# Performance work log

Hardware: AMD Instinct MI355X
Metric: run time of the kernel (lower is better)

Reference implementation:

```python
import jax, jax.numpy as jnp
import numpy as np

B, N, D, H = 8, 1024, 768, 12
HD = D // H  # head_dim = 64


def setup_inputs() -> dict:
    key = jax.random.key(0)
    ks = jax.random.split(key, 7)
    s = 1.0 / np.sqrt(D)  # xavier-ish scale for weights
    return {
        "x1": jax.random.normal(ks[0], (B, N, D), dtype=jnp.float32),
        "x2": jax.random.normal(ks[1], (B, N, D), dtype=jnp.float32),
        "Wq": jax.random.normal(ks[2], (D, D), dtype=jnp.float32) * s,
        "Wk": jax.random.normal(ks[3], (D, D), dtype=jnp.float32) * s,
        "Wv": jax.random.normal(ks[4], (D, D), dtype=jnp.float32) * s,
        "Wo": jax.random.normal(ks[5], (D, D), dtype=jnp.float32) * s,
        "bo": jnp.zeros((D,), dtype=jnp.float32),
    }


def _heads(x):
    # (B, N, D) -> (B, H, N, HD)
    return x.reshape(B, -1, H, HD).transpose(0, 2, 1, 3)


def reference(x1, x2, Wq, Wk, Wv, Wo, bo):
    scale = 1.0 / jnp.sqrt(jnp.asarray(HD, x1.dtype))
    q1 = _heads(x1 @ Wq.T)               # (B,H,N,HD)
    k1 = _heads(x1 @ Wk.T)
    v1 = _heads(x1 @ Wv.T)
    k2 = _heads(x2 @ Wk.T)
    v2 = _heads(x2 @ Wv.T)
    kc = jnp.concatenate([k1, k2], axis=2)   # (B,H,2N,HD)
    vc = jnp.concatenate([v1, v2], axis=2)
    attn = jnp.einsum('bhnd,bhmd->bhnm', q1, kc) * scale  # (B,H,N,2N)
    attn = jax.nn.softmax(attn, axis=-1)
    out = jnp.einsum('bhnm,bhmd->bhnd', attn, vc)          # (B,H,N,HD)
    out = out.transpose(0, 2, 1, 3).reshape(B, N, D)
    return out @ Wo.T + bo
```

## Files before the change

kernel.cpp:

```cpp
#include <hip/hip_runtime.h>


typedef __bf16 bf16x8 __attribute__((ext_vector_type(8)));
typedef float  f32x4  __attribute__((ext_vector_type(4)));
typedef unsigned int u32x4 __attribute__((ext_vector_type(4)));
typedef short  s16x4  __attribute__((ext_vector_type(4)));

__device__ __forceinline__ unsigned short bf16bits(float f) {
    return __builtin_bit_cast(unsigned short, (__bf16)f);
}
__device__ __forceinline__ unsigned pk2(float a, float b) {
    return (unsigned)bf16bits(a) | ((unsigned)bf16bits(b) << 16);
}
__device__ __forceinline__ bf16x8 asbf(u32x4 v) {
    return __builtin_bit_cast(bf16x8, v);
}
__device__ __forceinline__ float fexp2(float x) {
#if __has_builtin(__builtin_amdgcn_exp2f)
    return __builtin_amdgcn_exp2f(x);
#else
    return exp2f(x);
#endif
}
__device__ __forceinline__ float frcp(float x) {
#if __has_builtin(__builtin_amdgcn_rcpf)
    return __builtin_amdgcn_rcpf(x);
#else
    return 1.0f / x;
#endif
}

#define MFMA32(a, b, c) __builtin_amdgcn_mfma_f32_16x16x32_bf16((a), (b), (c), 0, 0, 0)

__global__ __launch_bounds__(256) void convert_all(
    const float* __restrict__ x1, const float* __restrict__ x2,
    const float* __restrict__ Wq, const float* __restrict__ Wk,
    const float* __restrict__ Wv, const float* __restrict__ Wo,
    unsigned short* __restrict__ x1b, unsigned short* __restrict__ x2b,
    unsigned short* __restrict__ Wcat, unsigned short* __restrict__ Wob)
{
    const float* src; unsigned short* dst; int n4;
    switch (blockIdx.y) {
        case 0:  src = x1; dst = x1b;            n4 = 1572864; break;
        case 1:  src = x2; dst = x2b;            n4 = 1572864; break;
        case 2:  src = Wq; dst = Wcat;           n4 = 147456;  break;
        case 3:  src = Wk; dst = Wcat +  589824; n4 = 147456;  break;
        case 4:  src = Wv; dst = Wcat + 1179648; n4 = 147456;  break;
        default: src = Wo; dst = Wob;            n4 = 147456;  break;
    }
    int i = blockIdx.x * 256 + threadIdx.x;
    if (i >= n4) return;
    float4 v = ((const float4*)src)[i];
    unsigned* o32 = (unsigned*)(dst + (size_t)i * 4);
    o32[0] = pk2(v.x, v.y);
    o32[1] = pk2(v.z, v.w);
}

__global__ __launch_bounds__(512, 2) void gemm256(
    const unsigned short* __restrict__ A1, const unsigned short* __restrict__ A2,
    const unsigned short* __restrict__ Wcat,
    unsigned short* __restrict__ dQ, unsigned short* __restrict__ dK,
    unsigned short* __restrict__ dV)
{
    __shared__ u32x4 smA[2][2048];
    __shared__ u32x4 smB[2][2048];

    const int tid  = threadIdx.x;
    const int lane = tid & 63;
    const int l15  = lane & 15;
    const int g    = lane >> 4;
    const int wid  = tid >> 6;
    const int wm   = wid >> 2;
    const int wn   = wid & 3;
    const int rb   = blockIdx.x;
    const int jb   = blockIdx.y;

    const bool br2 = (jb >= 9);
    const unsigned short* A  = br2 ? A2 : A1;
    const unsigned short* Bw = br2 ? (Wcat + 589824) : Wcat;
    const int jcol = br2 ? (jb - 9) : jb;

    f32x4 acc[8][4] = {};

#define GSTAGE256(KT, BO)                                                            \
    {                                                                                \
        int kt_ = (KT);                                                              \
        _Pragma("unroll")                                                            \
        for (int c_ = 0; c_ < 4; ++c_) {                                             \
            int i_   = c_ * 512 + tid;                                               \
            int row_ = i_ >> 3;                                                      \
            int gs_  = (i_ & 7) ^ (row_ & 7);                                        \
            const unsigned short* sa = A +                                           \
                (size_t)(rb * 256 + row_) * 768 + kt_ * 64 + gs_ * 8;                \
            __builtin_amdgcn_global_load_lds(                                        \
                (const __attribute__((address_space(1))) void*)sa,                   \
                (__attribute__((address_space(3))) void*)(smA[BO] + c_ * 512 + wid * 64), \
                16, 0, 0);                                                           \
            const unsigned short* sb = Bw +                                          \
                (size_t)(jcol * 256 + row_) * 768 + kt_ * 64 + gs_ * 8;              \
            __builtin_amdgcn_global_load_lds(                                        \
                (const __attribute__((address_space(1))) void*)sb,                   \
                (__attribute__((address_space(3))) void*)(smB[BO] + c_ * 512 + wid * 64), \
                16, 0, 0);                                                           \
        }                                                                            \
    }

    GSTAGE256(0, 0)
    asm volatile("s_waitcnt vmcnt(0)" ::: "memory");
    __builtin_amdgcn_s_barrier();

    for (int kt = 0; kt < 12; ++kt) {
        const int bufc = kt & 1;
        const u32x4* bA = smA[bufc];
        const u32x4* bB = smB[bufc];
        bf16x8 af[4], bfr[4];

        if (kt < 11) GSTAGE256(kt + 1, bufc ^ 1)
#pragma unroll
        for (int n = 0; n < 4; ++n) {
            int row = wn * 64 + n * 16 + l15;
            bfr[n] = asbf(bB[row * 8 + (g ^ (row & 7))]);
        }
#pragma unroll
        for (int m = 0; m < 4; ++m) {
            int row = wm * 128 + m * 16 + l15;
            af[m] = asbf(bA[row * 8 + (g ^ (row & 7))]);
        }
        __builtin_amdgcn_s_barrier();
        __builtin_amdgcn_sched_barrier(0);
        __builtin_amdgcn_s_setprio(1);
#pragma unroll
        for (int m = 0; m < 4; ++m)
#pragma unroll
            for (int n = 0; n < 4; ++n)
                acc[m][n] = MFMA32(af[m], bfr[n], acc[m][n]);
        __builtin_amdgcn_s_setprio(0);
        __builtin_amdgcn_s_barrier();

#pragma unroll
        for (int m = 0; m < 4; ++m) {
            int row = wm * 128 + 64 + m * 16 + l15;
            af[m] = asbf(bA[row * 8 + (g ^ (row & 7))]);
        }
        __builtin_amdgcn_s_barrier();
        __builtin_amdgcn_sched_barrier(0);
        __builtin_amdgcn_s_setprio(1);
#pragma unroll
        for (int m = 0; m < 4; ++m)
#pragma unroll
            for (int n = 0; n < 4; ++n)
                acc[4 + m][n] = MFMA32(af[m], bfr[n], acc[4 + m][n]);
        __builtin_amdgcn_s_setprio(0);
        __builtin_amdgcn_s_barrier();

#pragma unroll
        for (int n = 0; n < 4; ++n) {
            int row = wn * 64 + n * 16 + l15;
            bfr[n] = asbf(bB[row * 8 + ((4 + g) ^ (row & 7))]);
        }
#pragma unroll
        for (int m = 0; m < 4; ++m) {
            int row = wm * 128 + m * 16 + l15;
            af[m] = asbf(bA[row * 8 + ((4 + g) ^ (row & 7))]);
        }
        __builtin_amdgcn_s_barrier();
        __builtin_amdgcn_sched_barrier(0);
        __builtin_amdgcn_s_setprio(1);
#pragma unroll
        for (int m = 0; m < 4; ++m)
#pragma unroll
            for (int n = 0; n < 4; ++n)
                acc[m][n] = MFMA32(af[m], bfr[n], acc[m][n]);
        __builtin_amdgcn_s_setprio(0);
        __builtin_amdgcn_s_barrier();

#pragma unroll
        for (int m = 0; m < 4; ++m) {
            int row = wm * 128 + 64 + m * 16 + l15;
            af[m] = asbf(bA[row * 8 + ((4 + g) ^ (row & 7))]);
        }
        __builtin_amdgcn_s_barrier();
        __builtin_amdgcn_sched_barrier(0);
        __builtin_amdgcn_s_setprio(1);
#pragma unroll
        for (int m = 0; m < 4; ++m)
#pragma unroll
            for (int n = 0; n < 4; ++n)
                acc[4 + m][n] = MFMA32(af[m], bfr[n], acc[4 + m][n]);
        __builtin_amdgcn_s_setprio(0);
        asm volatile("s_waitcnt vmcnt(0)" ::: "memory");
        __builtin_amdgcn_s_barrier();
    }
#undef GSTAGE256

    const int rloc = wm * 128 + g * 4;
    const int cloc = wn * 64 + l15;
    const int seg  = jcol / 3;
    const int segq = br2 ? seg + 3 : seg;
    const int cseg = (jcol - seg * 3) * 256;
#pragma unroll
    for (int mf = 0; mf < 8; ++mf) {
#pragma unroll
        for (int n = 0; n < 4; ++n) {
            int r0 = rb * 256 + rloc + mf * 16;
            int cl = cseg + cloc + n * 16;
            int b = r0 >> 10, nn = r0 & 1023;
            int h = cl >> 6, hd = cl & 63;
            if (segq == 0) {
#pragma unroll
                for (int reg = 0; reg < 4; ++reg)
                    dQ[((size_t)(b * 12 + h) * 1024 + nn + reg) * 64 + hd] =
                        bf16bits(acc[mf][n][reg] * 0.18033688f);
            } else if (segq == 1 || segq == 3) {
                size_t koff = (segq == 3) ? 1024 : 0;
#pragma unroll
                for (int reg = 0; reg < 4; ++reg)
                    dK[((size_t)(b * 12 + h) * 2048 + koff + nn + reg) * 64 + hd] =
                        bf16bits(acc[mf][n][reg]);
            } else {
                size_t koff = (segq == 4) ? 1024 : 0;
                uint2 w;
                w.x = pk2(acc[mf][n][0], acc[mf][n][1]);
                w.y = pk2(acc[mf][n][2], acc[mf][n][3]);
                *(uint2*)(dV + ((size_t)(b * 12 + h) * 64 + hd) * 2048 +
                          koff + nn) = w;
            }
        }
    }
}

__global__ __launch_bounds__(256) void gemm_out(
    const unsigned short* __restrict__ A, const unsigned short* __restrict__ Bw,
    float* __restrict__ dO, const float* __restrict__ bias)
{
    __shared__ u32x4 smA[2048];
    __shared__ u32x4 smB[2048];

    const int tid  = threadIdx.x;
    const int lane = tid & 63;
    const int l15  = lane & 15;
    const int g    = lane >> 4;
    const int wid  = tid >> 6;
    const int rb   = blockIdx.x;
    const int jb   = blockIdx.y;
    const int wr   = (wid >> 1) * 64;
    const int wc   = (wid & 1) * 64;

    f32x4 acc[4][4] = {};

#define GSTAGE(KT, BO)                                                               \
    {                                                                                \
        int kt_ = (KT);                                                              \
        _Pragma("unroll")                                                            \
        for (int c_ = 0; c_ < 4; ++c_) {                                             \
            int i_   = (wid + c_ * 4) * 64 + lane;                                   \
            int row_ = i_ >> 3;                                                      \
            int gs_  = (i_ & 7) ^ (row_ & 7);                                        \
            const unsigned short* sa = A +                                           \
                (size_t)(rb * 128 + row_) * 768 + kt_ * 64 + gs_ * 8;                \
            __builtin_amdgcn_global_load_lds(                                        \
                (const __attribute__((address_space(1))) void*)sa,                   \
                (__attribute__((address_space(3))) void*)(smA + (BO) + (wid + c_ * 4) * 64), \
                16, 0, 0);                                                           \
            const unsigned short* sb = Bw +                                          \
                (size_t)(jb * 128 + row_) * 768 + kt_ * 64 + gs_ * 8;                \
            __builtin_amdgcn_global_load_lds(                                        \
                (const __attribute__((address_space(1))) void*)sb,                   \
                (__attribute__((address_space(3))) void*)(smB + (BO) + (wid + c_ * 4) * 64), \
                16, 0, 0);                                                           \
        }                                                                            \
    }

    GSTAGE(0, 0)

    for (int kt = 0; kt < 12; ++kt) {
        __builtin_amdgcn_s_barrier();
        if (kt < 11) {
            GSTAGE(kt + 1, ((kt + 1) & 1) << 10)
            asm volatile("s_waitcnt vmcnt(8)" ::: "memory");
        } else {
            asm volatile("s_waitcnt vmcnt(0)" ::: "memory");
        }
        __builtin_amdgcn_s_barrier();
        __builtin_amdgcn_sched_barrier(0);

        const u32x4* bA = smA + ((kt & 1) << 10);
        const u32x4* bB = smB + ((kt & 1) << 10);

#pragma unroll
        for (int kk = 0; kk < 2; ++kk) {
            bf16x8 af[4], bfr[4];
#pragma unroll
            for (int m = 0; m < 4; ++m) {
                int row = wr + m * 16 + l15;
                af[m] = asbf(bA[row * 8 + ((kk * 4 + g) ^ (row & 7))]);
            }
#pragma unroll
            for (int n = 0; n < 4; ++n) {
                int row = wc + n * 16 + l15;
                bfr[n] = asbf(bB[row * 8 + ((kk * 4 + g) ^ (row & 7))]);
            }
#pragma unroll
            for (int m = 0; m < 4; ++m)
#pragma unroll
                for (int n = 0; n < 4; ++n)
                    acc[m][n] = MFMA32(af[m], bfr[n], acc[m][n]);
        }
    }
#undef GSTAGE

    const int rloc = wr + g * 4;
    const int cloc = wc + l15;
#pragma unroll
    for (int m = 0; m < 4; ++m)
#pragma unroll
        for (int n = 0; n < 4; ++n) {
            int r0 = rb * 128 + rloc + m * 16;
            int c  = jb * 128 + cloc + n * 16;
#pragma unroll
            for (int reg = 0; reg < 4; ++reg)
                dO[(size_t)(r0 + reg) * 768 + c] = acc[m][n][reg] + bias[c];
        }
}

__global__ __launch_bounds__(256, 3) void attn_k(
    const unsigned short* __restrict__ Q, const unsigned short* __restrict__ K,
    const unsigned short* __restrict__ Vt, unsigned short* __restrict__ AO)
{
    __shared__ u32x4 sK[1536];
    __shared__ u32x4 sV[1536];

    const int tid  = threadIdx.x;
    const int lane = tid & 63;
    const int g    = lane >> 4;
    const int l15  = lane & 15;
    const int wid  = tid >> 6;
    const int bh   = blockIdx.x;
    const int q0   = blockIdx.y * 128;

    const unsigned short* Qh = Q  + (size_t)bh * (1024 * 64);
    const unsigned short* Kh = K  + (size_t)bh * (2048 * 64);
    const unsigned short* Vh = Vt + (size_t)bh * (64 * 2048);

    bf16x8 qf[2][2];
#pragma unroll
    for (int m = 0; m < 2; ++m)
#pragma unroll
        for (int kk = 0; kk < 2; ++kk)
            qf[m][kk] = *(const bf16x8*)(Qh +
                (size_t)(q0 + wid * 32 + m * 16 + l15) * 64 + kk * 32 + g * 8);

    f32x4 o[4][2] = {};
    float lr0 = 0.f, lr1 = 0.f;

#define STAGE_TILE(T, DOFF)                                                          \
    {                                                                                \
        int t_ = (T);                                                                \
        _Pragma("unroll")                                                            \
        for (int c_ = 0; c_ < 2; ++c_) {                                             \
            int i_   = (wid + c_ * 4) * 64 + lane;                                   \
            int row_ = i_ >> 3;                                                      \
            int gsK_ = (i_ & 7) ^ ((row_ & 3) | ((row_ >> 1) & 4));                  \
            int gsV_ = (i_ & 7) ^ (row_ & 7);                                        \
            const unsigned short* srcK_ = Kh + ((size_t)t_ * 64 + row_) * 64 + gsK_ * 8; \
            __builtin_amdgcn_global_load_lds(                                        \
                (const __attribute__((address_space(1))) void*)srcK_,               \
                (__attribute__((address_space(3))) void*)(sK + (DOFF) + (wid + c_ * 4) * 64), \
                16, 0, 0);                                                           \
            const unsigned short* srcV_ = Vh + (size_t)row_ * 2048 + t_ * 64 + gsV_ * 8; \
            __builtin_amdgcn_global_load_lds(                                        \
                (const __attribute__((address_space(1))) void*)srcV_,               \
                (__attribute__((address_space(3))) void*)(sV + (DOFF) + (wid + c_ * 4) * 64), \
                16, 0, 0);                                                           \
        }                                                                            \
    }

    STAGE_TILE(0, 0)
    STAGE_TILE(1, 512)

    for (int t = 0; t < 32; ++t) {
        if (t < 31) { asm volatile("s_waitcnt vmcnt(4)" ::: "memory"); }
        else        { asm volatile("s_waitcnt vmcnt(0)" ::: "memory"); }
        __builtin_amdgcn_s_barrier();
        if (t < 30) {
            STAGE_TILE(t + 2, ((t + 2) % 3) * 512)
        }
        __builtin_amdgcn_sched_barrier(0);

        const u32x4* sKb = sK + (t % 3) * 512;
        const u32x4* sVb = sV + (t % 3) * 512;

        f32x4 s[4][2] = {};
        __builtin_amdgcn_s_setprio(1);
#pragma unroll
        for (int kk = 0; kk < 2; ++kk) {
            bf16x8 kf[4];
#pragma unroll
            for (int n = 0; n < 4; ++n) {
                int rowp = ((n & 1) << 5) + ((l15 >> 2) << 3) +
                           (((n >> 1) & 1) << 2) + (l15 & 3);
                kf[n] = asbf(sKb[rowp * 8 + ((kk * 4 + g) ^ (l15 & 7))]);
            }
#pragma unroll
            for (int n = 0; n < 4; ++n)
#pragma unroll
                for (int m = 0; m < 2; ++m)
                    s[n][m] = MFMA32(kf[n], qf[m][kk], s[n][m]);
        }
        __builtin_amdgcn_s_setprio(0);

        float sum0 = 0.f, sum1 = 0.f;
        s16x4 p16[4][2];
#pragma unroll
        for (int n = 0; n < 4; ++n) {
            float p00 = fexp2(s[n][0][0]), p01 = fexp2(s[n][0][1]);
            float p02 = fexp2(s[n][0][2]), p03 = fexp2(s[n][0][3]);
            float p10 = fexp2(s[n][1][0]), p11 = fexp2(s[n][1][1]);
            float p12 = fexp2(s[n][1][2]), p13 = fexp2(s[n][1][3]);
            sum0 += (p00 + p01) + (p02 + p03);
            sum1 += (p10 + p11) + (p12 + p13);
            p16[n][0] = (s16x4){ (short)bf16bits(p00), (short)bf16bits(p01),
                                 (short)bf16bits(p02), (short)bf16bits(p03) };
            p16[n][1] = (s16x4){ (short)bf16bits(p10), (short)bf16bits(p11),
                                 (short)bf16bits(p12), (short)bf16bits(p13) };
        }
        lr0 += sum0; lr1 += sum1;

        __builtin_amdgcn_s_setprio(1);
#pragma unroll
        for (int kk = 0; kk < 2; ++kk) {
            bf16x8 pf[2];
#pragma unroll
            for (int m = 0; m < 2; ++m)
                pf[m] = __builtin_bit_cast(bf16x8,
                    __builtin_shufflevector(p16[kk][m], p16[kk + 2][m],
                                            0, 1, 2, 3, 4, 5, 6, 7));
#pragma unroll
            for (int v = 0; v < 4; ++v) {
                int row = v * 16 + l15;
                bf16x8 vf = asbf(sVb[row * 8 + ((kk * 4 + g) ^ (row & 7))]);
#pragma unroll
                for (int m = 0; m < 2; ++m)
                    o[v][m] = MFMA32(vf, pf[m], o[v][m]);
            }
        }
        __builtin_amdgcn_s_setprio(0);
    }

    lr0 += __shfl_xor(lr0, 16); lr0 += __shfl_xor(lr0, 32);
    lr1 += __shfl_xor(lr1, 16); lr1 += __shfl_xor(lr1, 32);
    const int b = bh / 12, h = bh % 12;
    float rl0 = frcp(lr0), rl1 = frcp(lr1);
#pragma unroll
    for (int m = 0; m < 2; ++m) {
        float rl = m ? rl1 : rl0;
        int q = q0 + wid * 32 + m * 16 + l15;
        unsigned short* dst = AO + (size_t)(b * 1024 + q) * 768 + h * 64 + g * 4;
#pragma unroll
        for (int v = 0; v < 4; ++v) {
            uint2 w;
            w.x = pk2(o[v][m][0] * rl, o[v][m][1] * rl);
            w.y = pk2(o[v][m][2] * rl, o[v][m][3] * rl);
            *(uint2*)(dst + v * 16) = w;
        }
    }
#undef STAGE_TILE
}

extern "C" void kernel_launch(void* const* d_in, const int* in_sizes, int n_in,
                              void* d_out, int out_size, void* d_ws, size_t ws_size,
                              hipStream_t stream)
{
    const float* x1 = (const float*)d_in[0];
    const float* x2 = (const float*)d_in[1];
    const float* Wq = (const float*)d_in[2];
    const float* Wk = (const float*)d_in[3];
    const float* Wv = (const float*)d_in[4];
    const float* Wo = (const float*)d_in[5];
    const float* bo = (const float*)d_in[6];

    unsigned short* Wcat = (unsigned short*)d_ws;
    unsigned short* Wob  = Wcat + 1769472;
    unsigned short* x1b  = Wob  + 589824;
    unsigned short* x2b  = x1b  + 6291456;
    unsigned short* Qb   = x2b  + 6291456;
    unsigned short* Kc   = Qb   + 6291456;
    unsigned short* Vt   = Kc   + 12582912;
    unsigned short* AO   = x1b;

    convert_all<<<dim3(6144, 6), 256, 0, stream>>>(x1, x2, Wq, Wk, Wv, Wo,
                                                   x1b, x2b, Wcat, Wob);

    gemm256<<<dim3(32, 15), 512, 0, stream>>>(x1b, x2b, Wcat, Qb, Kc, Vt);

    attn_k<<<dim3(96, 8), 256, 0, stream>>>(Qb, Kc, Vt, AO);

    gemm_out<<<dim3(64, 6), 256, 0, stream>>>(AO, Wob, (float*)d_out, bo);
}
```

Measured before the change: 164.3 us.

## Deepen QKV GEMM pipeline to 4-stage K=32 buffers and remap blocks for XCD locality

The projection GEMM now uses four smaller shared-memory buffers with a K-step of 32 instead of two with K-step 64. It prefetches two steps ahead and issues the A and B loads separately between MFMA phases, using partial vmcnt waits so several loads stay in flight and fewer barriers sit in the inner loop. The launch grid is flattened to 1D, with a remap that groups consecutive tiles on the same XCD for better L2 reuse. This costs twice as many loop iterations and relies on careful vmcnt accounting to stay correct.

```diff
diff --git a/kernel.cpp b/kernel.cpp
--- a/kernel.cpp
+++ b/kernel.cpp
@@ -62,8 +62,8 @@
     unsigned short* __restrict__ dQ, unsigned short* __restrict__ dK,
     unsigned short* __restrict__ dV)
 {
-    __shared__ u32x4 smA[2][2048];
-    __shared__ u32x4 smB[2][2048];
+    __shared__ u32x4 smA[4][1024];
+    __shared__ u32x4 smB[4][1024];
 
     const int tid  = threadIdx.x;
     const int lane = tid & 63;
@@ -72,8 +72,10 @@
     const int wid  = tid >> 6;
     const int wm   = wid >> 2;
     const int wn   = wid & 3;
-    const int rb   = blockIdx.x;
-    const int jb   = blockIdx.y;
+
+    const int wg   = (blockIdx.x & 7) * 60 + (blockIdx.x >> 3);
+    const int rb   = wg & 31;
+    const int jb   = wg >> 5;
 
     const bool br2 = (jb >= 9);
     const unsigned short* A  = br2 ? A2 : A1;
@@ -82,51 +84,61 @@
 
     f32x4 acc[8][4] = {};
 
-#define GSTAGE256(KT, BO)                                                            \
+#define STG_A(KT, BUF)                                                               \
     {                                                                                \
         int kt_ = (KT);                                                              \
         _Pragma("unroll")                                                            \
-        for (int c_ = 0; c_ < 4; ++c_) {                                             \
+        for (int c_ = 0; c_ < 2; ++c_) {                                             \
             int i_   = c_ * 512 + tid;                                               \
-            int row_ = i_ >> 3;                                                      \
-            int gs_  = (i_ & 7) ^ (row_ & 7);                                        \
+            int row_ = i_ >> 2;                                                      \
+            int gs_  = (i_ & 3) ^ (row_ & 3);                                        \
             const unsigned short* sa = A +                                           \
-                (size_t)(rb * 256 + row_) * 768 + kt_ * 64 + gs_ * 8;                \
+                (size_t)(rb * 256 + row_) * 768 + kt_ * 32 + gs_ * 8;                \
             __builtin_amdgcn_global_load_lds(                                        \
                 (const __attribute__((address_space(1))) void*)sa,                   \
-                (__attribute__((address_space(3))) void*)(smA[BO] + c_ * 512 + wid * 64), \
-                16, 0, 0);                                                           \
+                (__attribute__((address_space(3))) void*)(smA[BUF] + c_ * 512 + wid * 64), \
+                16, 0, 0);                                                           \
+        }                                                                            \
+    }
+#define STG_B(KT, BUF)                                                               \
+    {                                                                                \
+        int kt_ = (KT);                                                              \
+        _Pragma("unroll")                                                            \
+        for (int c_ = 0; c_ < 2; ++c_) {                                             \
+            int i_   = c_ * 512 + tid;                                               \
+            int row_ = i_ >> 2;                                                      \
+            int gs_  = (i_ & 3) ^ (row_ & 3);                                        \
             const unsigned short* sb = Bw +                                          \
-                (size_t)(jcol * 256 + row_) * 768 + kt_ * 64 + gs_ * 8;              \
+                (size_t)(jcol * 256 + row_) * 768 + kt_ * 32 + gs_ * 8;              \
             __builtin_amdgcn_global_load_lds(                                        \
                 (const __attribute__((address_space(1))) void*)sb,                   \
-                (__attribute__((address_space(3))) void*)(smB[BO] + c_ * 512 + wid * 64), \
+                (__attribute__((address_space(3))) void*)(smB[BUF] + c_ * 512 + wid * 64), \
                 16, 0, 0);                                                           \
         }                                                                            \
     }
 
-    GSTAGE256(0, 0)
-    asm volatile("s_waitcnt vmcnt(0)" ::: "memory");
+    STG_A(0, 0) STG_B(0, 0)
+    STG_A(1, 1) STG_B(1, 1)
+    asm volatile("s_waitcnt vmcnt(4)" ::: "memory");
     __builtin_amdgcn_s_barrier();
 
-    for (int kt = 0; kt < 12; ++kt) {
-        const int bufc = kt & 1;
-        const u32x4* bA = smA[bufc];
-        const u32x4* bB = smB[bufc];
+    for (int kt = 0; kt < 24; ++kt) {
+        const int buf = kt & 3;
+        const u32x4* bA = smA[buf];
+        const u32x4* bB = smB[buf];
         bf16x8 af[4], bfr[4];
 
-        if (kt < 11) GSTAGE256(kt + 1, bufc ^ 1)
 #pragma unroll
         for (int n = 0; n < 4; ++n) {
             int row = wn * 64 + n * 16 + l15;
-            bfr[n] = asbf(bB[row * 8 + (g ^ (row & 7))]);
+            bfr[n] = asbf(bB[row * 4 + (g ^ (row & 3))]);
         }
 #pragma unroll
         for (int m = 0; m < 4; ++m) {
             int row = wm * 128 + m * 16 + l15;
-            af[m] = asbf(bA[row * 8 + (g ^ (row & 7))]);
-        }
-        __builtin_amdgcn_s_barrier();
+            af[m] = asbf(bA[row * 4 + (g ^ (row & 3))]);
+        }
+        if (kt < 22) STG_A(kt + 2, (kt + 2) & 3)
         __builtin_amdgcn_sched_barrier(0);
         __builtin_amdgcn_s_setprio(1);
 #pragma unroll
@@ -140,9 +152,9 @@
 #pragma unroll
         for (int m = 0; m < 4; ++m) {
             int row = wm * 128 + 64 + m * 16 + l15;
-            af[m] = asbf(bA[row * 8 + (g ^ (row & 7))]);
-        }
-        __builtin_amdgcn_s_barrier();
+            af[m] = asbf(bA[row * 4 + (g ^ (row & 3))]);
+        }
+        if (kt < 22) STG_B(kt + 2, (kt + 2) & 3)
         __builtin_amdgcn_sched_barrier(0);
         __builtin_amdgcn_s_setprio(1);
 #pragma unroll
@@ -151,47 +163,12 @@
             for (int n = 0; n < 4; ++n)
                 acc[4 + m][n] = MFMA32(af[m], bfr[n], acc[4 + m][n]);
         __builtin_amdgcn_s_setprio(0);
+        if (kt < 22)      { asm volatile("s_waitcnt vmcnt(4)" ::: "memory"); }
+        else if (kt == 22){ asm volatile("s_waitcnt vmcnt(0)" ::: "memory"); }
         __builtin_amdgcn_s_barrier();
-
-#pragma unroll
-        for (int n = 0; n < 4; ++n) {
-            int row = wn * 64 + n * 16 + l15;
-            bfr[n] = asbf(bB[row * 8 + ((4 + g) ^ (row & 7))]);
-        }
-#pragma unroll
-        for (int m = 0; m < 4; ++m) {
-            int row = wm * 128 + m * 16 + l15;
-            af[m] = asbf(bA[row * 8 + ((4 + g) ^ (row & 7))]);
-        }
-        __builtin_amdgcn_s_barrier();
-        __builtin_amdgcn_sched_barrier(0);
-        __builtin_amdgcn_s_setprio(1);
-#pragma unroll
-        for (int m = 0; m < 4; ++m)
-#pragma unroll
-            for (int n = 0; n < 4; ++n)
-                acc[m][n] = MFMA32(af[m], bfr[n], acc[m][n]);
-        __builtin_amdgcn_s_setprio(0);
-        __builtin_amdgcn_s_barrier();
-
-#pragma unroll
-        for (int m = 0; m < 4; ++m) {
-            int row = wm * 128 + 64 + m * 16 + l15;
-            af[m] = asbf(bA[row * 8 + ((4 + g) ^ (row & 7))]);
-        }
-        __builtin_amdgcn_s_barrier();
-        __builtin_amdgcn_sched_barrier(0);
-        __builtin_amdgcn_s_setprio(1);
-#pragma unroll
-        for (int m = 0; m < 4; ++m)
-#pragma unroll
-            for (int n = 0; n < 4; ++n)
-                acc[4 + m][n] = MFMA32(af[m], bfr[n], acc[4 + m][n]);
-        __builtin_amdgcn_s_setprio(0);
-        asm volatile("s_waitcnt vmcnt(0)" ::: "memory");
-        __builtin_amdgcn_s_barrier();
-    }
-#undef GSTAGE256
+    }
+#undef STG_A
+#undef STG_B
 
     const int rloc = wm * 128 + g * 4;
     const int cloc = wn * 64 + l15;
@@ -491,7 +468,7 @@
     convert_all<<<dim3(6144, 6), 256, 0, stream>>>(x1, x2, Wq, Wk, Wv, Wo,
                                                    x1b, x2b, Wcat, Wob);
 
-    gemm256<<<dim3(32, 15), 512, 0, stream>>>(x1b, x2b, Wcat, Qb, Kc, Vt);
+    gemm256<<<dim3(480), 512, 0, stream>>>(x1b, x2b, Wcat, Qb, Kc, Vt);
 
     attn_k<<<dim3(96, 8), 256, 0, stream>>>(Qb, Kc, Vt, AO);
 
```

Result: no change. 163.8 us (-0.3%).
